# Kernel tuning notes

Measured on AMD Instinct MI355X. Metric: run time of the kernel, lower is better.

Reference implementation:

```python
import jax, jax.numpy as jnp
import numpy as np

N, E = 50000, 800000
IN_DIM, EMBED, EDGE_DIM, H = 16, 32, 4, 4
C1 = 2 * EMBED          # per-head out dim of conv1 (64)
C2 = EMBED              # per-head out dim of conv2 (32)
NEG_SLOPE = 0.2


def _p(key, shape, scale=0.1):
    return jax.random.normal(key, shape, dtype=jnp.float32) * scale


def setup_inputs() -> dict:
    key = jax.random.key(0)
    ks = jax.random.split(key, 16)
    x = jax.random.normal(ks[0], (N, IN_DIM), dtype=jnp.float32)
    edge_index = jax.random.randint(ks[1], (2, E), 0, N, dtype=jnp.int32)
    edge_attr = jax.random.normal(ks[2], (E, EDGE_DIM), dtype=jnp.float32)
    params = {
        # conv1: in 16 -> heads*64
        "W1": _p(ks[3], (IN_DIM, H * C1)),
        "We1": _p(ks[4], (EDGE_DIM, H * C1)),
        "as1": _p(ks[5], (H, C1)),
        "ad1": _p(ks[6], (H, C1)),
        "ae1": _p(ks[7], (H, C1)),
        "b1": jnp.zeros((H * C1,), jnp.float32),
        # conv2: in heads*C1=256 -> heads*32
        "W2": _p(ks[8], (H * C1, H * C2)),
        "We2": _p(ks[9], (EDGE_DIM, H * C2)),
        "as2": _p(ks[10], (H, C2)),
        "ad2": _p(ks[11], (H, C2)),
        "ae2": _p(ks[12], (H, C2)),
        "b2": jnp.zeros((H * C2,), jnp.float32),
    }
    return {"x": x, "edge_index": edge_index, "edge_attr": edge_attr, **params}


def gat_layer(x, edge_index, edge_attr, Wx, We, a_src, a_dst, a_edge, bias, heads, ch):
    """PyG GATConv with edge_dim, concat=True, add_self_loops (fill_value='mean')."""
    n = x.shape[0]
    src, dst = edge_index[0], edge_index[1]
    # self-loop edge_attr = per-node mean of incoming edge attrs (PyG fill_value='mean')
    cnt = jax.ops.segment_sum(jnp.ones((edge_attr.shape[0],), edge_attr.dtype), dst, num_segments=n)
    loop_ea = jax.ops.segment_sum(edge_attr, dst, num_segments=n) / jnp.maximum(cnt, 1.0)[:, None]
    loop = jnp.arange(n, dtype=src.dtype)
    src = jnp.concatenate([src, loop])
    dst = jnp.concatenate([dst, loop])
    ea = jnp.concatenate([edge_attr, loop_ea], axis=0)

    xh = (x @ Wx).reshape(n, heads, ch)             # [N,H,C]
    eh = (ea @ We).reshape(-1, heads, ch)           # [E+N,H,C]
    a_s = jnp.einsum('nhc,hc->nh', xh, a_src)
    a_d = jnp.einsum('nhc,hc->nh', xh, a_dst)
    a_e = jnp.einsum('ehc,hc->eh', eh, a_edge)
    logit = jax.nn.leaky_relu(a_s[src] + a_d[dst] + a_e, NEG_SLOPE)  # [E+N,H]
    # segment softmax over edges sharing destination node
    m = jax.ops.segment_max(logit, dst, num_segments=n)
    ex = jnp.exp(logit - m[dst])
    den = jax.ops.segment_sum(ex, dst, num_segments=n)
    alpha = ex / den[dst]
    out = jax.ops.segment_sum(alpha[..., None] * xh[src], dst, num_segments=n)  # [N,H,C]
    return out.reshape(n, heads * ch) + bias


def reference(x, edge_index, edge_attr, W1, We1, as1, ad1, ae1, b1,
              W2, We2, as2, ad2, ae2, b2):
    h = gat_layer(x, edge_index, edge_attr, W1, We1, as1, ad1, ae1, b1, H, C1)
    h = jax.nn.relu(h)
    return gat_layer(h, edge_index, edge_attr, W2, We2, as2, ad2, ae2, b2, H, C2)
```

## Files before the change

kernel.cpp:

```cpp
#include <hip/hip_runtime.h>
#include <hip/hip_bf16.h>


#define NEG_SLOPE 0.2f

__device__ __forceinline__ float lrelu(float v) { return v > 0.f ? v : NEG_SLOPE * v; }

__global__ void ve_kernel(const float* __restrict__ We1, const float* __restrict__ ae1,
                          const float* __restrict__ We2, const float* __restrict__ ae2,
                          float* __restrict__ Ve) {
    int t = threadIdx.x;
    if (t < 16) {
        int d = t >> 2, h = t & 3;
        float s = 0.f;
        for (int c = 0; c < 64; ++c) s += We1[d * 256 + h * 64 + c] * ae1[h * 64 + c];
        Ve[t] = s;
    } else if (t < 32) {
        int tt = t - 16;
        int d = tt >> 2, h = tt & 3;
        float s = 0.f;
        for (int c = 0; c < 32; ++c) s += We2[d * 128 + h * 32 + c] * ae2[h * 32 + c];
        Ve[16 + tt] = s;
    }
}

__global__ void hist_kernel(const int* __restrict__ dst, int* __restrict__ cnt, int E) {
    int e = blockIdx.x * blockDim.x + threadIdx.x;
    if (e >= E) return;
    atomicAdd(&cnt[dst[e]], 1);
}

__global__ void blockscan_kernel(const int* __restrict__ cnt, int* __restrict__ off,
                                 int* __restrict__ bsum, int n) {
    __shared__ int wsum[8];
    int b = blockIdx.x, tid = threadIdx.x;
    int i = b * 512 + tid;
    int lane = tid & 63, w = tid >> 6;
    int v = (i < n) ? cnt[i] : 0;
    int s = v;
#pragma unroll
    for (int o = 1; o < 64; o <<= 1) {
        int t = __shfl_up(s, o, 64);
        if (lane >= o) s += t;
    }
    if (lane == 63) wsum[w] = s;
    __syncthreads();
    if (tid == 0) {
        int run = 0;
#pragma unroll
        for (int k = 0; k < 8; ++k) { int t = wsum[k]; wsum[k] = run; run += t; }
        bsum[b] = run;
    }
    __syncthreads();
    s += wsum[w];
    if (i < n) off[i + 1] = s;
}

__global__ void bsumscan_kernel(int* __restrict__ bsum, int nb) {
    if (threadIdx.x == 0) {
        int run = 0;
        for (int k = 0; k < nb; ++k) { int t = bsum[k]; bsum[k] = run; run += t; }
    }
}

__global__ void scanadd_kernel(const int* __restrict__ bsum, int* __restrict__ off, int n) {
    int i = blockIdx.x * 512 + threadIdx.x;
    if (i == 0) off[0] = 0;
    if (i < n) off[i + 1] += bsum[blockIdx.x];
}

__global__ void scatter_kernel(const int* __restrict__ src, const int* __restrict__ dst,
                               const float* __restrict__ ea, const int* __restrict__ off,
                               int* __restrict__ fill, const float* __restrict__ Ve,
                               int* __restrict__ src_sorted, float* __restrict__ ae1s,
                               float* __restrict__ ae2s, int E) {
    int e = blockIdx.x * blockDim.x + threadIdx.x;
    if (e >= E) return;
    int d = dst[e];
    int pos = off[d] + atomicAdd(&fill[d], 1);
    src_sorted[pos] = src[e];
    float e4[4];
#pragma unroll
    for (int k = 0; k < 4; ++k) e4[k] = ea[e * 4 + k];
#pragma unroll
    for (int h = 0; h < 4; ++h) {
        float s1 = 0.f, s2 = 0.f;
#pragma unroll
        for (int k = 0; k < 4; ++k) { s1 += e4[k] * Ve[k * 4 + h]; s2 += e4[k] * Ve[16 + k * 4 + h]; }
        ae1s[pos * 4 + h] = s1;
        ae2s[pos * 4 + h] = s2;
    }
}

__global__ void aeloop_kernel(const int* __restrict__ off,
                              const float* __restrict__ ae1s, const float* __restrict__ ae2s,
                              float* __restrict__ aeloop1, float* __restrict__ aeloop2, int n) {
    int t = blockIdx.x * blockDim.x + threadIdx.x;
    int node = t >> 3, k = t & 7;
    if (node >= n) return;
    int beg = off[node], end = off[node + 1];
    int deg = end - beg;
    float inv = 1.f / (float)(deg > 0 ? deg : 1);
    const float* srcp = (k < 4) ? ae1s : ae2s;
    int h = k & 3;
    float s = 0.f;
    for (int i = beg; i < end; ++i) s += srcp[(size_t)i * 4 + h];
    float* dstp = (k < 4) ? aeloop1 : aeloop2;
    dstp[(size_t)node * 4 + h] = s * inv;
}

__global__ void gemm1_kernel(const float* __restrict__ x, const float* __restrict__ W1,
                             const float* __restrict__ as1, const float* __restrict__ ad1,
                             __hip_bfloat16* __restrict__ xh1, float* __restrict__ a_s,
                             float* __restrict__ a_d, int N) {
    constexpr int R = 8;
    __shared__ float sx[R * 16];
    int n0 = blockIdx.x * R;
    int j = threadIdx.x;
    for (int idx = j; idx < R * 16; idx += 256) {
        int r = idx >> 4, k = idx & 15;
        int nn = n0 + r;
        sx[idx] = (nn < N) ? x[nn * 16 + k] : 0.f;
    }
    __syncthreads();
    float acc[R];
#pragma unroll
    for (int r = 0; r < R; ++r) acc[r] = 0.f;
#pragma unroll
    for (int k = 0; k < 16; ++k) {
        float w = W1[k * 256 + j];
#pragma unroll
        for (int r = 0; r < R; ++r) acc[r] += sx[r * 16 + k] * w;
    }
    float as = as1[j], ad = ad1[j];
    int h = j >> 6;
#pragma unroll
    for (int r = 0; r < R; ++r) {
        int nn = n0 + r;
        if (nn < N) xh1[(size_t)nn * 256 + j] = __float2bfloat16(acc[r]);
        float va = acc[r] * as, vd = acc[r] * ad;
#pragma unroll
        for (int o = 32; o > 0; o >>= 1) {
            va += __shfl_xor(va, o, 64);
            vd += __shfl_xor(vd, o, 64);
        }
        if ((j & 63) == 0 && nn < N) { a_s[nn * 4 + h] = va; a_d[nn * 4 + h] = vd; }
    }
}

__global__ void gemm2_kernel(const float* __restrict__ h1, const float* __restrict__ W2,
                             const float* __restrict__ as2, const float* __restrict__ ad2,
                             __hip_bfloat16* __restrict__ xh2, float* __restrict__ a_s,
                             float* __restrict__ a_d, int N) {
    constexpr int R = 16;
    __shared__ float sh[R * 256];
    int n0 = blockIdx.x * R;
    int j = threadIdx.x;
    for (int idx = j; idx < R * 256; idx += 128) {
        int r = idx >> 8, k = idx & 255;
        int nn = n0 + r;
        sh[idx] = (nn < N) ? h1[(size_t)nn * 256 + k] : 0.f;
    }
    __syncthreads();
    float acc[R];
#pragma unroll
    for (int r = 0; r < R; ++r) acc[r] = 0.f;
    for (int k = 0; k < 256; ++k) {
        float w = W2[k * 128 + j];
#pragma unroll
        for (int r = 0; r < R; ++r) acc[r] += sh[r * 256 + k] * w;
    }
    float as = as2[j], ad = ad2[j];
    int h = j >> 5;
#pragma unroll
    for (int r = 0; r < R; ++r) {
        int nn = n0 + r;
        if (nn < N) xh2[(size_t)nn * 128 + j] = __float2bfloat16(acc[r]);
        float va = acc[r] * as, vd = acc[r] * ad;
#pragma unroll
        for (int o = 16; o > 0; o >>= 1) {
            va += __shfl_xor(va, o, 32);
            vd += __shfl_xor(vd, o, 32);
        }
        if ((j & 31) == 0 && nn < N) { a_s[nn * 4 + h] = va; a_d[nn * 4 + h] = vd; }
    }
}

template <int CT, int C>
__global__ __launch_bounds__(CT) void agg_kernel(
        const int* __restrict__ off, const int* __restrict__ srcs,
        const float* __restrict__ aes, const float* __restrict__ aeloop,
        const float* __restrict__ a_s, const float* __restrict__ a_d,
        const __hip_bfloat16* __restrict__ xh, const float* __restrict__ bias,
        float* __restrict__ out, int relu) {
    constexpr int CAP = 512;
    constexpr int NW  = CT / 64;
    constexpr int TPG = CT / 4;
    __shared__ int   s_src[CAP];
    __shared__ float s_lg[CAP * 4];
    __shared__ float s_wred[NW * 4];
    __shared__ float s_m[4];
    __shared__ float s_den[4];

    int n = blockIdx.x;
    int j = threadIdx.x;
    int beg = off[n], end = off[n + 1];
    int deg = end - beg;
    int tot = deg + 1;
    int h = j / C;

    const float4 ad4 = *(const float4*)&a_d[(size_t)n * 4];

    if (tot <= CAP) {
        for (int idx = j; idx < tot; idx += CT) {
            int s; float4 ae;
            if (idx < deg) {
                s  = srcs[beg + idx];
                ae = *(const float4*)&aes[(size_t)(beg + idx) * 4];
            } else {
                s  = n;
                ae = *(const float4*)&aeloop[(size_t)n * 4];
            }
            s_src[idx] = s;
            float4 as4 = *(const float4*)&a_s[(size_t)s * 4];
            s_lg[idx * 4 + 0] = lrelu(as4.x + ad4.x + ae.x);
            s_lg[idx * 4 + 1] = lrelu(as4.y + ad4.y + ae.y);
            s_lg[idx * 4 + 2] = lrelu(as4.z + ad4.z + ae.z);
            s_lg[idx * 4 + 3] = lrelu(as4.w + ad4.w + ae.w);
        }
        __syncthreads();
        int lane = j & 63, w = j >> 6;
        int g = j & 3, r = j >> 2;
        float m = -3.4e38f;
        for (int i = r; i < tot; i += TPG) m = fmaxf(m, s_lg[i * 4 + g]);
#pragma unroll
        for (int o = 4; o < 64; o <<= 1) m = fmaxf(m, __shfl_xor(m, o, 64));
        if (lane < 4) s_wred[w * 4 + lane] = m;
        __syncthreads();
        if (j < 4) {
            float mm = s_wred[j];
            for (int ww = 1; ww < NW; ++ww) mm = fmaxf(mm, s_wred[ww * 4 + j]);
            s_m[j] = mm;
        }
        __syncthreads();
        float mh = s_m[g];
        float den = 0.f;
        for (int i = r; i < tot; i += TPG) {
            float e = expf(s_lg[i * 4 + g] - mh);
            s_lg[i * 4 + g] = e;
            den += e;
        }
#pragma unroll
        for (int o = 4; o < 64; o <<= 1) den += __shfl_xor(den, o, 64);
        if (lane < 4) s_wred[w * 4 + lane] = den;
        __syncthreads();
        if (j < 4) {
            float dd = s_wred[j];
            for (int ww = 1; ww < NW; ++ww) dd += s_wred[ww * 4 + j];
            s_den[j] = dd;
        }
        __syncthreads();
        float invden = 1.f / s_den[h];
        float acc = 0.f;
        int i = 0;
        for (; i + 1 < tot; i += 2) {
            float w0 = s_lg[i * 4 + h], w1 = s_lg[(i + 1) * 4 + h];
            int   s0 = s_src[i],        s1 = s_src[i + 1];
            float x0 = __bfloat162float(xh[(size_t)s0 * CT + j]);
            float x1 = __bfloat162float(xh[(size_t)s1 * CT + j]);
            acc += w0 * x0;
            acc += w1 * x1;
        }
        if (i < tot) acc += s_lg[i * 4 + h] * __bfloat162float(xh[(size_t)s_src[i] * CT + j]);
        float o2 = acc * invden + bias[j];
        if (relu) o2 = fmaxf(o2, 0.f);
        out[(size_t)n * CT + j] = o2;
    } else {
        float adh = ((const float*)&ad4)[h];
        float lself = lrelu(a_s[(size_t)n * 4 + h] + adh + aeloop[(size_t)n * 4 + h]);
        float m = lself;
        for (int i2 = beg; i2 < end; ++i2) {
            int s = srcs[i2];
            float lg = lrelu(a_s[(size_t)s * 4 + h] + adh + aes[(size_t)i2 * 4 + h]);
            m = fmaxf(m, lg);
        }
        float ex = expf(lself - m);
        float den = ex;
        float acc = ex * __bfloat162float(xh[(size_t)n * CT + j]);
        for (int i2 = beg; i2 < end; ++i2) {
            int s = srcs[i2];
            float lg = lrelu(a_s[(size_t)s * 4 + h] + adh + aes[(size_t)i2 * 4 + h]);
            float e2 = expf(lg - m);
            den += e2;
            acc += e2 * __bfloat162float(xh[(size_t)s * CT + j]);
        }
        float o2 = acc / den + bias[j];
        if (relu) o2 = fmaxf(o2, 0.f);
        out[(size_t)n * CT + j] = o2;
    }
}

extern "C" void kernel_launch(void* const* d_in, const int* in_sizes, int n_in,
                              void* d_out, int out_size, void* d_ws, size_t ws_size,
                              hipStream_t stream) {
    const float* x   = (const float*)d_in[0];
    const int*   ei  = (const int*)d_in[1];
    const float* ea  = (const float*)d_in[2];
    const float* W1  = (const float*)d_in[3];
    const float* We1 = (const float*)d_in[4];
    const float* as1 = (const float*)d_in[5];
    const float* ad1 = (const float*)d_in[6];
    const float* ae1 = (const float*)d_in[7];
    const float* b1  = (const float*)d_in[8];
    const float* W2  = (const float*)d_in[9];
    const float* We2 = (const float*)d_in[10];
    const float* as2 = (const float*)d_in[11];
    const float* ad2 = (const float*)d_in[12];
    const float* ae2 = (const float*)d_in[13];
    const float* b2  = (const float*)d_in[14];
    float* out = (float*)d_out;

    const int N = in_sizes[0] / 16;
    const int E = in_sizes[1] / 2;
    const int* srcp = ei;
    const int* dstp = ei + E;
    const int NB = (N + 511) / 512;

    char* w = (char*)d_ws;
    size_t o = 0;
    auto alloc = [&](size_t bytes) -> void* {
        void* p = w + o;
        o += (bytes + 255) & ~(size_t)255;
        return p;
    };
    int*   cnt     = (int*)alloc((size_t)N * 4);
    int*   fill    = (int*)alloc((size_t)N * 4);
    size_t zero_bytes = o;
    int*   off_    = (int*)alloc((size_t)(N + 1) * 4);
    int*   bsum    = (int*)alloc((size_t)NB * 4);
    float* Ve      = (float*)alloc(32 * 4);
    float* aeloop1 = (float*)alloc((size_t)N * 16);
    float* aeloop2 = (float*)alloc((size_t)N * 16);
    float* a_s1    = (float*)alloc((size_t)N * 16);
    float* a_d1    = (float*)alloc((size_t)N * 16);
    float* a_s2    = (float*)alloc((size_t)N * 16);
    float* a_d2    = (float*)alloc((size_t)N * 16);
    int*   src_s   = (int*)alloc((size_t)E * 4);
    float* ae1s    = (float*)alloc((size_t)E * 16);
    float* ae2s    = (float*)alloc((size_t)E * 16);
    __hip_bfloat16* xh1 = (__hip_bfloat16*)alloc((size_t)N * 256 * 2);
    float* h1      = (float*)alloc((size_t)N * 256 * 4);
    __hip_bfloat16* xh2 = xh1;

    hipMemsetAsync(d_ws, 0, zero_bytes, stream);
    ve_kernel<<<1, 64, 0, stream>>>(We1, ae1, We2, ae2, Ve);
    hist_kernel<<<(E + 255) / 256, 256, 0, stream>>>(dstp, cnt, E);
    blockscan_kernel<<<NB, 512, 0, stream>>>(cnt, off_, bsum, N);
    bsumscan_kernel<<<1, 64, 0, stream>>>(bsum, NB);
    scanadd_kernel<<<NB, 512, 0, stream>>>(bsum, off_, N);
    scatter_kernel<<<(E + 255) / 256, 256, 0, stream>>>(srcp, dstp, ea, off_, fill, Ve,
                                                        src_s, ae1s, ae2s, E);
    aeloop_kernel<<<(N * 8 + 255) / 256, 256, 0, stream>>>(off_, ae1s, ae2s,
                                                           aeloop1, aeloop2, N);
    gemm1_kernel<<<(N + 7) / 8, 256, 0, stream>>>(x, W1, as1, ad1, xh1, a_s1, a_d1, N);
    agg_kernel<256, 64><<<N, 256, 0, stream>>>(off_, src_s, ae1s, aeloop1, a_s1, a_d1,
                                               xh1, b1, h1, 1);
    gemm2_kernel<<<(N + 15) / 16, 128, 0, stream>>>(h1, W2, as2, ad2, xh2, a_s2, a_d2, N);
    agg_kernel<128, 32><<<N, 128, 0, stream>>>(off_, src_s, ae2s, aeloop2, a_s2, a_d2,
                                               xh2, b2, out, 0);
}
```

Before: 603.8 us.

## Process two bf16 channels per thread in layer-1 aggregation, shrink LDS cap

The layer-1 aggregation kernel now runs with 128 threads per node, and each thread loads a packed pair of bf16 features as one 32-bit word. This halves the gather instruction count and the softmax-phase thread overhead. The weighted-sum loop is unrolled by four with manual bf16-to-float bit conversion in both layers. The shared-memory edge cap drops from 512 to 96 to raise occupancy, which sends high-degree nodes (rare at average degree 16) to the slow serial fallback path.

```diff
diff --git a/kernel.cpp b/kernel.cpp
--- a/kernel.cpp
+++ b/kernel.cpp
@@ -5,6 +5,8 @@
 #define NEG_SLOPE 0.2f
 
 __device__ __forceinline__ float lrelu(float v) { return v > 0.f ? v : NEG_SLOPE * v; }
+__device__ __forceinline__ float bf_lo(unsigned v) { return __uint_as_float(v << 16); }
+__device__ __forceinline__ float bf_hi(unsigned v) { return __uint_as_float(v & 0xffff0000u); }
 
 __global__ void ve_kernel(const float* __restrict__ We1, const float* __restrict__ ae1,
                           const float* __restrict__ We2, const float* __restrict__ ae2,
@@ -186,14 +188,16 @@
     }
 }
 
-template <int CT, int C>
+template <int CT, int CH>
 __global__ __launch_bounds__(CT) void agg_kernel(
         const int* __restrict__ off, const int* __restrict__ srcs,
         const float* __restrict__ aes, const float* __restrict__ aeloop,
         const float* __restrict__ a_s, const float* __restrict__ a_d,
         const __hip_bfloat16* __restrict__ xh, const float* __restrict__ bias,
         float* __restrict__ out, int relu) {
-    constexpr int CAP = 512;
+    constexpr int CPT = CH / CT;
+    constexpr int C   = CH / 4;
+    constexpr int CAP = 96;
     constexpr int NW  = CT / 64;
     constexpr int TPG = CT / 4;
     __shared__ int   s_src[CAP];
@@ -207,7 +211,7 @@
     int beg = off[n], end = off[n + 1];
     int deg = end - beg;
     int tot = deg + 1;
-    int h = j / C;
+    int h = (j * CPT) / C;
 
     const float4 ad4 = *(const float4*)&a_d[(size_t)n * 4];
 
@@ -261,42 +265,80 @@
         }
         __syncthreads();
         float invden = 1.f / s_den[h];
-        float acc = 0.f;
-        int i = 0;
-        for (; i + 1 < tot; i += 2) {
-            float w0 = s_lg[i * 4 + h], w1 = s_lg[(i + 1) * 4 + h];
-            int   s0 = s_src[i],        s1 = s_src[i + 1];
-            float x0 = __bfloat162float(xh[(size_t)s0 * CT + j]);
-            float x1 = __bfloat162float(xh[(size_t)s1 * CT + j]);
-            acc += w0 * x0;
-            acc += w1 * x1;
-        }
-        if (i < tot) acc += s_lg[i * 4 + h] * __bfloat162float(xh[(size_t)s_src[i] * CT + j]);
-        float o2 = acc * invden + bias[j];
-        if (relu) o2 = fmaxf(o2, 0.f);
-        out[(size_t)n * CT + j] = o2;
+        if constexpr (CPT == 2) {
+            const unsigned* xu = (const unsigned*)xh;
+            constexpr int CHW = CH / 2;
+            float a0 = 0.f, a1 = 0.f;
+            int i = 0;
+            for (; i + 4 <= tot; i += 4) {
+                float w0 = s_lg[(i+0)*4+h], w1 = s_lg[(i+1)*4+h];
+                float w2 = s_lg[(i+2)*4+h], w3 = s_lg[(i+3)*4+h];
+                int s0 = s_src[i+0], s1 = s_src[i+1], s2 = s_src[i+2], s3 = s_src[i+3];
+                unsigned v0 = xu[(size_t)s0 * CHW + j];
+                unsigned v1 = xu[(size_t)s1 * CHW + j];
+                unsigned v2 = xu[(size_t)s2 * CHW + j];
+                unsigned v3 = xu[(size_t)s3 * CHW + j];
+                a0 += w0 * bf_lo(v0); a1 += w0 * bf_hi(v0);
+                a0 += w1 * bf_lo(v1); a1 += w1 * bf_hi(v1);
+                a0 += w2 * bf_lo(v2); a1 += w2 * bf_hi(v2);
+                a0 += w3 * bf_lo(v3); a1 += w3 * bf_hi(v3);
+            }
+            for (; i < tot; ++i) {
+                float ww = s_lg[i * 4 + h];
+                unsigned v = xu[(size_t)s_src[i] * CHW + j];
+                a0 += ww * bf_lo(v); a1 += ww * bf_hi(v);
+            }
+            float2 bb = ((const float2*)bias)[j];
+            float o0 = a0 * invden + bb.x;
+            float o1 = a1 * invden + bb.y;
+            if (relu) { o0 = fmaxf(o0, 0.f); o1 = fmaxf(o1, 0.f); }
+            ((float2*)&out[(size_t)n * CH])[j] = make_float2(o0, o1);
+        } else {
+            const unsigned short* xs = (const unsigned short*)xh;
+            float a0 = 0.f;
+            int i = 0;
+            for (; i + 4 <= tot; i += 4) {
+                float w0 = s_lg[(i+0)*4+h], w1 = s_lg[(i+1)*4+h];
+                float w2 = s_lg[(i+2)*4+h], w3 = s_lg[(i+3)*4+h];
+                int s0 = s_src[i+0], s1 = s_src[i+1], s2 = s_src[i+2], s3 = s_src[i+3];
+                float x0 = __uint_as_float((unsigned)xs[(size_t)s0 * CH + j] << 16);
+                float x1 = __uint_as_float((unsigned)xs[(size_t)s1 * CH + j] << 16);
+                float x2 = __uint_as_float((unsigned)xs[(size_t)s2 * CH + j] << 16);
+                float x3 = __uint_as_float((unsigned)xs[(size_t)s3 * CH + j] << 16);
+                a0 += w0 * x0; a0 += w1 * x1; a0 += w2 * x2; a0 += w3 * x3;
+            }
+            for (; i < tot; ++i)
+                a0 += s_lg[i * 4 + h] *
+                      __uint_as_float((unsigned)xs[(size_t)s_src[i] * CH + j] << 16);
+            float o2 = a0 * invden + bias[j];
+            if (relu) o2 = fmaxf(o2, 0.f);
+            out[(size_t)n * CH + j] = o2;
+        }
     } else {
-        float adh = ((const float*)&ad4)[h];
-        float lself = lrelu(a_s[(size_t)n * 4 + h] + adh + aeloop[(size_t)n * 4 + h]);
-        float m = lself;
-        for (int i2 = beg; i2 < end; ++i2) {
-            int s = srcs[i2];
-            float lg = lrelu(a_s[(size_t)s * 4 + h] + adh + aes[(size_t)i2 * 4 + h]);
-            m = fmaxf(m, lg);
-        }
-        float ex = expf(lself - m);
-        float den = ex;
-        float acc = ex * __bfloat162float(xh[(size_t)n * CT + j]);
-        for (int i2 = beg; i2 < end; ++i2) {
-            int s = srcs[i2];
-            float lg = lrelu(a_s[(size_t)s * 4 + h] + adh + aes[(size_t)i2 * 4 + h]);
-            float e2 = expf(lg - m);
-            den += e2;
-            acc += e2 * __bfloat162float(xh[(size_t)s * CT + j]);
-        }
-        float o2 = acc / den + bias[j];
-        if (relu) o2 = fmaxf(o2, 0.f);
-        out[(size_t)n * CT + j] = o2;
+        for (int c = j * CPT; c < (j + 1) * CPT; ++c) {
+            int hh = c / C;
+            float adh = ((const float*)&ad4)[hh];
+            float lself = lrelu(a_s[(size_t)n * 4 + hh] + adh + aeloop[(size_t)n * 4 + hh]);
+            float m = lself;
+            for (int i2 = beg; i2 < end; ++i2) {
+                int s = srcs[i2];
+                float lg = lrelu(a_s[(size_t)s * 4 + hh] + adh + aes[(size_t)i2 * 4 + hh]);
+                m = fmaxf(m, lg);
+            }
+            float ex = expf(lself - m);
+            float den = ex;
+            float acc = ex * __bfloat162float(xh[(size_t)n * CH + c]);
+            for (int i2 = beg; i2 < end; ++i2) {
+                int s = srcs[i2];
+                float lg = lrelu(a_s[(size_t)s * 4 + hh] + adh + aes[(size_t)i2 * 4 + hh]);
+                float e2 = expf(lg - m);
+                den += e2;
+                acc += e2 * __bfloat162float(xh[(size_t)s * CH + c]);
+            }
+            float o2 = acc / den + bias[c];
+            if (relu) o2 = fmaxf(o2, 0.f);
+            out[(size_t)n * CH + c] = o2;
+        }
     }
 }
 
@@ -363,9 +405,9 @@
     aeloop_kernel<<<(N * 8 + 255) / 256, 256, 0, stream>>>(off_, ae1s, ae2s,
                                                            aeloop1, aeloop2, N);
     gemm1_kernel<<<(N + 7) / 8, 256, 0, stream>>>(x, W1, as1, ad1, xh1, a_s1, a_d1, N);
-    agg_kernel<256, 64><<<N, 256, 0, stream>>>(off_, src_s, ae1s, aeloop1, a_s1, a_d1,
-                                               xh1, b1, h1, 1);
+    agg_kernel<128, 256><<<N, 128, 0, stream>>>(off_, src_s, ae1s, aeloop1, a_s1, a_d1,
+                                                xh1, b1, h1, 1);
     gemm2_kernel<<<(N + 15) / 16, 128, 0, stream>>>(h1, W2, as2, ad2, xh2, a_s2, a_d2, N);
-    agg_kernel<128, 32><<<N, 128, 0, stream>>>(off_, src_s, ae2s, aeloop2, a_s2, a_d2,
-                                               xh2, b2, out, 0);
-}
+    agg_kernel<128, 128><<<N, 128, 0, stream>>>(off_, src_s, ae2s, aeloop2, a_s2, a_d2,
+                                                xh2, b2, out, 0);
+}
```

After: 537.8 us. 10.9% less time.
